# Kernel optimization log

Measured on AMD Instinct MI355X. Metric: run time of the kernel, lower is better.

## Reference

```python
import jax, jax.numpy as jnp
import numpy as np

WS = 7
NUM_HEADS = 12
DIM = 384
HEAD_DIM = DIM // NUM_HEADS
SCALE = HEAD_DIM ** -0.5


def _rel_pos_index(ws: int) -> jnp.ndarray:
    coords = np.stack(np.meshgrid(np.arange(ws), np.arange(ws), indexing='ij'))  # (2, ws, ws)
    cf = coords.reshape(2, -1)                       # (2, ws*ws)
    rel = cf[:, :, None] - cf[:, None, :]            # (2, N, N)
    rel = rel.transpose(1, 2, 0).copy()              # (N, N, 2)
    rel[..., 0] += ws - 1
    rel[..., 1] += ws - 1
    rel[..., 0] *= 2 * ws - 1
    return jnp.asarray(rel.sum(-1))                  # (N, N) int indices into bias table


REL_IDX = _rel_pos_index(WS)


def setup_inputs() -> dict:
    key = jax.random.key(0)
    ks = jax.random.split(key, 7)
    BW, N, C = 4096, WS * WS, DIM
    num_win = 64
    return {
        'x': jax.random.normal(ks[0], (BW, N, C), jnp.float32),
        'mask': jax.random.normal(ks[1], (num_win, N, N), jnp.float32),
        'qkv_w': jax.random.normal(ks[2], (3 * C, C), jnp.float32) * 0.02,
        'qkv_b': jax.random.normal(ks[3], (3 * C,), jnp.float32) * 0.02,
        'proj_w': jax.random.normal(ks[4], (C, C), jnp.float32) * 0.02,
        'proj_b': jax.random.normal(ks[5], (C,), jnp.float32) * 0.02,
        'bias_table': jax.random.normal(ks[6], ((2 * WS - 1) ** 2, NUM_HEADS), jnp.float32) * 0.02,
    }


def reference(x, mask, qkv_w, qkv_b, proj_w, proj_b, bias_table):
    BW, N, C = x.shape
    H, hd = NUM_HEADS, HEAD_DIM
    # QKV projection: (BW, N, 3C) -> (3, BW, H, N, hd)
    qkv = (x @ qkv_w.T + qkv_b).reshape(BW, N, 3, H, hd).transpose(2, 0, 3, 1, 4)
    q, k, v = qkv[0], qkv[1], qkv[2]
    attn = jnp.einsum('bhnd,bhmd->bhnm', q, k) * SCALE  # (BW, H, N, N)
    bias = bias_table[REL_IDX]                          # (N, N, H)
    attn = attn + bias.transpose(2, 0, 1)[None]
    num_win = mask.shape[0]
    attn = attn.reshape(BW // num_win, num_win, H, N, N) + mask[None, :, None]
    attn = attn.reshape(BW, H, N, N)
    attn = jax.nn.softmax(attn, axis=-1)
    out = jnp.einsum('bhnm,bhmd->bhnd', attn, v)        # (BW, H, N, hd)
    out = out.transpose(0, 2, 1, 3).reshape(BW, N, C)
    return out @ proj_w.T + proj_b
```

## Files before the change

kernel.cpp:

```cpp
#include <hip/hip_runtime.h>

typedef unsigned short u16;
typedef unsigned int u32;
typedef __attribute__((ext_vector_type(8))) short short8;
typedef __attribute__((ext_vector_type(4))) float floatx4;

#define SCALE_Q 0.17677669529663687f

__device__ __forceinline__ u16 f2bf(float f) {
  u32 u = __float_as_uint(f);
  u = (u + 0x7fffu + ((u >> 16) & 1u)) >> 16;
  return (u16)u;
}

__device__ __forceinline__ void gload_lds16(const void* g, void* l) {
  __builtin_amdgcn_global_load_lds(
      (const __attribute__((address_space(1))) u32*)g,
      (__attribute__((address_space(3))) u32*)l, 16, 0, 0);
}

__device__ __forceinline__ floatx4 mfma16(short8 a, short8 b, floatx4 c) {
  return __builtin_amdgcn_mfma_f32_16x16x32_bf16(a, b, c, 0, 0, 0);
}

__global__ void cast_w_kernel(const float* __restrict__ qkv_w,
                              const float* __restrict__ proj_w,
                              u16* __restrict__ wb1, u16* __restrict__ wb2) {
  int idx = blockIdx.x * 256 + threadIdx.x;
  wb1[idx] = f2bf(qkv_w[idx]);
  if (idx < 147456) wb2[idx] = f2bf(proj_w[idx]);
}

__global__ __launch_bounds__(256) void cast_x_kernel(const float* __restrict__ x,
                                                     u16* __restrict__ xb) {
  const size_t i = ((size_t)blockIdx.x * 256 + threadIdx.x) * 8;
  const float4 f0 = *(const float4*)(x + i);
  const float4 f1 = *(const float4*)(x + i + 4);
  uint4 pk;
  pk.x = (u32)f2bf(f0.x) | ((u32)f2bf(f0.y) << 16);
  pk.y = (u32)f2bf(f0.z) | ((u32)f2bf(f0.w) << 16);
  pk.z = (u32)f2bf(f1.x) | ((u32)f2bf(f1.y) << 16);
  pk.w = (u32)f2bf(f1.z) | ((u32)f2bf(f1.w) << 16);
  *(uint4*)(xb + i) = pk;
}

__global__ void comb_kernel(const float* __restrict__ bias_table,
                            const float* __restrict__ mask,
                            float* __restrict__ comb) {
  int wh = blockIdx.x;
  int w = wh / 12, h = wh - w * 12;
  float* dst = comb + (size_t)wh * 4096;
  for (int e = threadIdx.x; e < 4096; e += 256) {
    int q = e >> 6, p = e & 63;
    float v;
    if (q >= 49) v = -1e30f;
    else if (p >= 49) v = 0.0f;
    else {
      int pi = p / 7, pj = p - pi * 7;
      int qi = q / 7, qj = q - qi * 7;
      int ridx = (pi - qi + 6) * 13 + (pj - qj + 6);
      v = bias_table[ridx * 12 + h] + mask[(size_t)w * 2401 + p * 49 + q];
    }
    dst[e] = v;
  }
}

__global__ __launch_bounds__(256) void qkv_gemm(const u16* __restrict__ A,
                                                const u16* __restrict__ B,
                                                const float* __restrict__ bias,
                                                u16* __restrict__ C) {
  __shared__ u16 As[2][4096];
  __shared__ u16 Bs[2][4096];
  const int tid = threadIdx.x;
  const int lane = tid & 63;
  const int wave = tid >> 6;
  const int l15 = lane & 15;
  const int quad = lane >> 4;
  const int wr = wave >> 1, wc = wave & 1;
  const u32 bid = blockIdx.x;
  const u32 xcd = bid & 7;
  const u32 slot = bid >> 3;
  const u32 grp = slot / 9;
  const u32 tn = slot - grp * 9;
  const u32 tm = xcd * 196 + grp;

  const int c0 = tid, c1 = tid + 256;
  const int m0 = c0 >> 2, kp0 = (c0 & 3) ^ ((m0 >> 1) & 3);
  const int m1 = c1 >> 2, kp1 = (c1 & 3) ^ ((m1 >> 1) & 3);
  const u16* Ab0 = A + (size_t)(tm * 128 + m0) * 384 + kp0 * 8;
  const u16* Ab1 = A + (size_t)(tm * 128 + m1) * 384 + kp1 * 8;
  const u16* Bb0 = B + (size_t)(tn * 128 + m0) * 384 + kp0 * 8;
  const u16* Bb1 = B + (size_t)(tn * 128 + m1) * 384 + kp1 * 8;
  const int ld0 = c0 * 8, ld1 = c1 * 8;

  floatx4 acc[4][4];
#pragma unroll
  for (int i = 0; i < 4; ++i)
#pragma unroll
    for (int j = 0; j < 4; ++j) acc[i][j] = (floatx4){0.f, 0.f, 0.f, 0.f};

#define QSTAGE(buf, k0)                       \
  do {                                        \
    gload_lds16(Ab0 + (k0), &As[buf][ld0]);   \
    gload_lds16(Ab1 + (k0), &As[buf][ld1]);   \
    gload_lds16(Bb0 + (k0), &Bs[buf][ld0]);   \
    gload_lds16(Bb1 + (k0), &Bs[buf][ld1]);   \
  } while (0)

  QSTAGE(0, 0);
  __syncthreads();

  const int xq = quad ^ ((l15 >> 1) & 3);
  const int abase = (wr * 64 + l15) * 32 + xq * 8;
  const int bbase = (wc * 64 + l15) * 32 + xq * 8;
  for (int kb = 0; kb < 12; ++kb) {
    const int cur = kb & 1;
    if (kb < 11) QSTAGE(cur ^ 1, (kb + 1) * 32);
    short8 af[4], bfr[4];
#pragma unroll
    for (int i = 0; i < 4; ++i)
      af[i] = *(const short8*)(&As[cur][abase + i * 512]);
#pragma unroll
    for (int i = 0; i < 4; ++i)
      bfr[i] = *(const short8*)(&Bs[cur][bbase + i * 512]);
#pragma unroll
    for (int mi = 0; mi < 4; ++mi)
#pragma unroll
      for (int ni = 0; ni < 4; ++ni)
        acc[mi][ni] = mfma16(af[mi], bfr[ni], acc[mi][ni]);
    if (kb < 11) __syncthreads();
  }
#undef QSTAGE

#pragma unroll
  for (int ni = 0; ni < 4; ++ni) {
    const int gbase = (int)tn * 128 + wc * 64 + ni * 16;
    const int which = gbase / 384;
    const int rem = gbase - which * 384;
    const int h = rem >> 5;
    const int db = rem & 31;
    const float bb = bias[gbase + l15];
    const float scale = (which == 0) ? SCALE_Q : 1.0f;
    u16* hp = C + ((size_t)which * 49152 + h) * 1568 + db + l15;
#pragma unroll
    for (int mi = 0; mi < 4; ++mi) {
      const int grow0 = (int)tm * 128 + wr * 64 + mi * 16 + quad * 4;
#pragma unroll
      for (int r = 0; r < 4; ++r) {
        const int grow = grow0 + r;
        const int b = grow / 49;
        const int tok = grow - b * 49;
        hp[(size_t)b * 18816 + tok * 32] = f2bf((acc[mi][ni][r] + bb) * scale);
      }
    }
  }
}

__global__ __launch_bounds__(64) void attn_kernel(const u16* __restrict__ qkv,
                                                  const float* __restrict__ comb,
                                                  u16* __restrict__ ao) {
  __shared__ uint4 smem4[864];
  u16* Ps = (u16*)smem4;
  u16* Vt = (u16*)((char*)smem4 + 9216);

  const int tid = threadIdx.x;
  const int l15 = tid & 15, quad = tid >> 4;
  const int bh = blockIdx.x;
  const int b = bh / 12, h = bh - b * 12;
  const int w = b & 63;

  const size_t hoff = (size_t)bh * 1568;
  const u16* qb = qkv + hoff;
  const u16* kbp = qkv + (size_t)49152 * 1568 + hoff;
  const u16* vb = qkv + (size_t)98304 * 1568 + hoff;

  short8 aq[4], bk[4];
  const short8 z8 = {0, 0, 0, 0, 0, 0, 0, 0};
#pragma unroll
  for (int i = 0; i < 3; ++i) {
    aq[i] = *(const short8*)(qb + (i * 16 + l15) * 32 + quad * 8);
    bk[i] = *(const short8*)(kbp + (i * 16 + l15) * 32 + quad * 8);
  }
  aq[3] = (l15 == 0) ? *(const short8*)(qb + 48 * 32 + quad * 8) : z8;
  bk[3] = (l15 == 0) ? *(const short8*)(kbp + 48 * 32 + quad * 8) : z8;

  const uint4 z = make_uint4(0u, 0u, 0u, 0u);
  for (int i = tid; i < 288; i += 64) smem4[576 + i] = z;

  for (int s0 = tid; s0 < 196; s0 += 64) {
    const int t = s0 >> 2, part = s0 & 3;
    const uint4 dv = *(const uint4*)(vb + t * 32 + part * 8);
    const int d0 = part * 8;
    const u32 vv[4] = {dv.x, dv.y, dv.z, dv.w};
#pragma unroll
    for (int j = 0; j < 4; ++j) {
      Vt[(d0 + 2 * j) * 72 + t] = (u16)(vv[j] & 0xffffu);
      Vt[(d0 + 2 * j + 1) * 72 + t] = (u16)(vv[j] >> 16);
    }
  }

  floatx4 s[4][4];
  const floatx4 z4 = (floatx4){0.f, 0.f, 0.f, 0.f};
  __builtin_amdgcn_s_setprio(1);
#pragma unroll
  for (int mi = 0; mi < 4; ++mi)
#pragma unroll
    for (int ni = 0; ni < 4; ++ni) s[mi][ni] = mfma16(aq[mi], bk[ni], z4);
  __builtin_amdgcn_s_setprio(0);

  const float* cb = comb + (size_t)(w * 12 + h) * 4096;
#pragma unroll
  for (int ni = 0; ni < 4; ++ni)
#pragma unroll
    for (int mi = 0; mi < 4; ++mi) {
      const float4 cv = *(const float4*)(cb + (ni * 16 + l15) * 64 + mi * 16 + quad * 4);
      s[mi][ni][0] += cv.x;
      s[mi][ni][1] += cv.y;
      s[mi][ni][2] += cv.z;
      s[mi][ni][3] += cv.w;
    }

  floatx4 mx[4], sm[4];
#pragma unroll
  for (int mi = 0; mi < 4; ++mi)
#pragma unroll
    for (int r = 0; r < 4; ++r)
      mx[mi][r] = fmaxf(fmaxf(s[mi][0][r], s[mi][1][r]), fmaxf(s[mi][2][r], s[mi][3][r]));
#pragma unroll
  for (int d = 1; d < 16; d <<= 1)
#pragma unroll
    for (int mi = 0; mi < 4; ++mi)
#pragma unroll
      for (int r = 0; r < 4; ++r)
        mx[mi][r] = fmaxf(mx[mi][r], __shfl_xor(mx[mi][r], d));
#pragma unroll
  for (int mi = 0; mi < 4; ++mi)
#pragma unroll
    for (int r = 0; r < 4; ++r) {
      float a = 0.f;
#pragma unroll
      for (int ni = 0; ni < 4; ++ni) {
        const float e = __expf(s[mi][ni][r] - mx[mi][r]);
        s[mi][ni][r] = e;
        a += e;
      }
      sm[mi][r] = a;
    }
#pragma unroll
  for (int d = 1; d < 16; d <<= 1)
#pragma unroll
    for (int mi = 0; mi < 4; ++mi)
#pragma unroll
      for (int r = 0; r < 4; ++r)
        sm[mi][r] += __shfl_xor(sm[mi][r], d);

#pragma unroll
  for (int mi = 0; mi < 4; ++mi)
#pragma unroll
    for (int r = 0; r < 4; ++r) {
      const float rinv = 1.0f / sm[mi][r];
      const int row = mi * 16 + quad * 4 + r;
#pragma unroll
      for (int ni = 0; ni < 4; ++ni)
        Ps[row * 72 + ni * 16 + l15] = f2bf(s[mi][ni][r] * rinv);
    }
  __syncthreads();

  floatx4 o[4][2];
#pragma unroll
  for (int mi = 0; mi < 4; ++mi)
#pragma unroll
    for (int ni = 0; ni < 2; ++ni) o[mi][ni] = z4;
#pragma unroll
  for (int kk = 0; kk < 2; ++kk) {
    short8 ap[4], bv[2];
#pragma unroll
    for (int mi = 0; mi < 4; ++mi)
      ap[mi] = *(const short8*)(Ps + (mi * 16 + l15) * 72 + kk * 32 + quad * 8);
#pragma unroll
    for (int ni = 0; ni < 2; ++ni)
      bv[ni] = *(const short8*)(Vt + (ni * 16 + l15) * 72 + kk * 32 + quad * 8);
    __builtin_amdgcn_s_setprio(1);
#pragma unroll
    for (int mi = 0; mi < 4; ++mi)
#pragma unroll
      for (int ni = 0; ni < 2; ++ni) o[mi][ni] = mfma16(ap[mi], bv[ni], o[mi][ni]);
    __builtin_amdgcn_s_setprio(0);
  }
#pragma unroll
  for (int mi = 0; mi < 4; ++mi)
#pragma unroll
    for (int r = 0; r < 4; ++r) {
      const int row = mi * 16 + quad * 4 + r;
      if (row < 49) {
        u16* dst = ao + (size_t)(b * 49 + row) * 384 + h * 32;
#pragma unroll
        for (int ni = 0; ni < 2; ++ni)
          dst[ni * 16 + l15] = f2bf(o[mi][ni][r]);
      }
    }
}

__global__ __launch_bounds__(256) void proj_gemm(const u16* __restrict__ A,
                                                 const u16* __restrict__ B,
                                                 const float* __restrict__ bias,
                                                 float* __restrict__ C) {
  __shared__ u16 As[2][4096];
  __shared__ u16 Bs[2][4096];
  const int tid = threadIdx.x;
  const int lane = tid & 63;
  const int wave = tid >> 6;
  const int l15 = lane & 15;
  const int quad = lane >> 4;
  const int wr = wave >> 1, wc = wave & 1;
  const u32 bid = blockIdx.x;
  const u32 xcd = bid & 7;
  const u32 slot = bid >> 3;
  const u32 grp = slot / 3;
  const u32 tn = slot - grp * 3;
  const u32 tm = xcd * 196 + grp;

  const int c0 = tid, c1 = tid + 256;
  const int m0 = c0 >> 2, kp0 = (c0 & 3) ^ ((m0 >> 1) & 3);
  const int m1 = c1 >> 2, kp1 = (c1 & 3) ^ ((m1 >> 1) & 3);
  const u16* Ab0 = A + (size_t)(tm * 128 + m0) * 384 + kp0 * 8;
  const u16* Ab1 = A + (size_t)(tm * 128 + m1) * 384 + kp1 * 8;
  const u16* Bb0 = B + (size_t)(tn * 128 + m0) * 384 + kp0 * 8;
  const u16* Bb1 = B + (size_t)(tn * 128 + m1) * 384 + kp1 * 8;
  const int ld0 = c0 * 8, ld1 = c1 * 8;

  floatx4 acc[4][4];
#pragma unroll
  for (int i = 0; i < 4; ++i)
#pragma unroll
    for (int j = 0; j < 4; ++j) acc[i][j] = (floatx4){0.f, 0.f, 0.f, 0.f};

#define PSTAGE(buf, k0)                       \
  do {                                        \
    gload_lds16(Ab0 + (k0), &As[buf][ld0]);   \
    gload_lds16(Ab1 + (k0), &As[buf][ld1]);   \
    gload_lds16(Bb0 + (k0), &Bs[buf][ld0]);   \
    gload_lds16(Bb1 + (k0), &Bs[buf][ld1]);   \
  } while (0)

  PSTAGE(0, 0);
  __syncthreads();

  const int xq = quad ^ ((l15 >> 1) & 3);
  const int abase = (wr * 64 + l15) * 32 + xq * 8;
  const int bbase = (wc * 64 + l15) * 32 + xq * 8;
  for (int kb = 0; kb < 12; ++kb) {
    const int cur = kb & 1;
    if (kb < 11) PSTAGE(cur ^ 1, (kb + 1) * 32);
    short8 af[4], bfr[4];
#pragma unroll
    for (int i = 0; i < 4; ++i)
      af[i] = *(const short8*)(&As[cur][abase + i * 512]);
#pragma unroll
    for (int i = 0; i < 4; ++i)
      bfr[i] = *(const short8*)(&Bs[cur][bbase + i * 512]);
#pragma unroll
    for (int mi = 0; mi < 4; ++mi)
#pragma unroll
      for (int ni = 0; ni < 4; ++ni)
        acc[mi][ni] = mfma16(af[mi], bfr[ni], acc[mi][ni]);
    if (kb < 11) __syncthreads();
  }
#undef PSTAGE

#pragma unroll
  for (int ni = 0; ni < 4; ++ni) {
    const int gcol = tn * 128 + wc * 64 + ni * 16 + l15;
    const float bb = bias[gcol];
#pragma unroll
    for (int mi = 0; mi < 4; ++mi) {
      const int grow0 = tm * 128 + wr * 64 + mi * 16 + quad * 4;
#pragma unroll
      for (int r = 0; r < 4; ++r)
        C[(size_t)(grow0 + r) * 384 + gcol] = acc[mi][ni][r] + bb;
    }
  }
}

extern "C" void kernel_launch(void* const* d_in, const int* in_sizes, int n_in,
                              void* d_out, int out_size, void* d_ws, size_t ws_size,
                              hipStream_t stream) {
  const float* x = (const float*)d_in[0];
  const float* mask = (const float*)d_in[1];
  const float* qkv_w = (const float*)d_in[2];
  const float* qkv_b = (const float*)d_in[3];
  const float* proj_w = (const float*)d_in[4];
  const float* proj_b = (const float*)d_in[5];
  const float* bias_table = (const float*)d_in[6];
  float* out = (float*)d_out;
  char* ws = (char*)d_ws;

  u16* wb1 = (u16*)(ws);
  u16* wb2 = (u16*)(ws + 884736);
  float* comb = (float*)(ws + 1179648);
  u16* qkvb = (u16*)(ws + 13762560);
  u16* ao = (u16*)(ws + 476184576);
  u16* xb = ao;

  hipLaunchKernelGGL(cast_w_kernel, dim3(1728), dim3(256), 0, stream, qkv_w, proj_w, wb1, wb2);
  hipLaunchKernelGGL(cast_x_kernel, dim3(37632), dim3(256), 0, stream, x, xb);
  hipLaunchKernelGGL(comb_kernel, dim3(768), dim3(256), 0, stream, bias_table, mask, comb);
  hipLaunchKernelGGL(qkv_gemm, dim3(14112), dim3(256), 0, stream, xb, wb1, qkv_b, qkvb);
  hipLaunchKernelGGL(attn_kernel, dim3(49152), dim3(64), 0, stream, qkvb, comb, ao);
  hipLaunchKernelGGL(proj_gemm, dim3(4704), dim3(256), 0, stream, ao, wb2, proj_b, out);
}
```

Baseline: 1.208 ms.

## Fuse window attention with output projection and single-buffer the QKV GEMM

The separate per-head attention kernel and the projection GEMM are replaced by one kernel per window. Its four waves each handle three heads, write the attention output into a shared-memory tile, then run the projection against weights read straight from global memory. This removes the global round trip of the attention output and one launch. In exchange it uses about 105KB of LDS with launch bounds of one block, so occupancy is low and the weight loads in the projection loop are poorly hidden. Separately, the QKV GEMM drops its double buffering for a single LDS buffer synchronised before and after compute, which halves its LDS but exposes load latency.

```diff
diff --git a/kernel.cpp b/kernel.cpp
--- a/kernel.cpp
+++ b/kernel.cpp
@@ -69,8 +69,8 @@
                                                 const u16* __restrict__ B,
                                                 const float* __restrict__ bias,
                                                 u16* __restrict__ C) {
-  __shared__ u16 As[2][4096];
-  __shared__ u16 Bs[2][4096];
+  __shared__ u16 As[4096];
+  __shared__ u16 Bs[4096];
   const int tid = threadIdx.x;
   const int lane = tid & 63;
   const int wave = tid >> 6;
@@ -99,38 +99,30 @@
 #pragma unroll
     for (int j = 0; j < 4; ++j) acc[i][j] = (floatx4){0.f, 0.f, 0.f, 0.f};
 
-#define QSTAGE(buf, k0)                       \
-  do {                                        \
-    gload_lds16(Ab0 + (k0), &As[buf][ld0]);   \
-    gload_lds16(Ab1 + (k0), &As[buf][ld1]);   \
-    gload_lds16(Bb0 + (k0), &Bs[buf][ld0]);   \
-    gload_lds16(Bb1 + (k0), &Bs[buf][ld1]);   \
-  } while (0)
-
-  QSTAGE(0, 0);
-  __syncthreads();
-
   const int xq = quad ^ ((l15 >> 1) & 3);
   const int abase = (wr * 64 + l15) * 32 + xq * 8;
   const int bbase = (wc * 64 + l15) * 32 + xq * 8;
   for (int kb = 0; kb < 12; ++kb) {
-    const int cur = kb & 1;
-    if (kb < 11) QSTAGE(cur ^ 1, (kb + 1) * 32);
+    const int k0 = kb * 32;
+    gload_lds16(Ab0 + k0, &As[ld0]);
+    gload_lds16(Ab1 + k0, &As[ld1]);
+    gload_lds16(Bb0 + k0, &Bs[ld0]);
+    gload_lds16(Bb1 + k0, &Bs[ld1]);
+    __syncthreads();
     short8 af[4], bfr[4];
 #pragma unroll
     for (int i = 0; i < 4; ++i)
-      af[i] = *(const short8*)(&As[cur][abase + i * 512]);
+      af[i] = *(const short8*)(&As[abase + i * 512]);
 #pragma unroll
     for (int i = 0; i < 4; ++i)
-      bfr[i] = *(const short8*)(&Bs[cur][bbase + i * 512]);
+      bfr[i] = *(const short8*)(&Bs[bbase + i * 512]);
 #pragma unroll
     for (int mi = 0; mi < 4; ++mi)
 #pragma unroll
       for (int ni = 0; ni < 4; ++ni)
         acc[mi][ni] = mfma16(af[mi], bfr[ni], acc[mi][ni]);
-    if (kb < 11) __syncthreads();
-  }
-#undef QSTAGE
+    __syncthreads();
+  }
 
 #pragma unroll
   for (int ni = 0; ni < 4; ++ni) {
@@ -156,229 +148,198 @@
   }
 }
 
-__global__ __launch_bounds__(64) void attn_kernel(const u16* __restrict__ qkv,
-                                                  const float* __restrict__ comb,
-                                                  u16* __restrict__ ao) {
-  __shared__ uint4 smem4[864];
-  u16* Ps = (u16*)smem4;
-  u16* Vt = (u16*)((char*)smem4 + 9216);
-
-  const int tid = threadIdx.x;
-  const int l15 = tid & 15, quad = tid >> 4;
-  const int bh = blockIdx.x;
-  const int b = bh / 12, h = bh - b * 12;
-  const int w = b & 63;
-
-  const size_t hoff = (size_t)bh * 1568;
-  const u16* qb = qkv + hoff;
-  const u16* kbp = qkv + (size_t)49152 * 1568 + hoff;
-  const u16* vb = qkv + (size_t)98304 * 1568 + hoff;
-
-  short8 aq[4], bk[4];
-  const short8 z8 = {0, 0, 0, 0, 0, 0, 0, 0};
-#pragma unroll
-  for (int i = 0; i < 3; ++i) {
-    aq[i] = *(const short8*)(qb + (i * 16 + l15) * 32 + quad * 8);
-    bk[i] = *(const short8*)(kbp + (i * 16 + l15) * 32 + quad * 8);
-  }
-  aq[3] = (l15 == 0) ? *(const short8*)(qb + 48 * 32 + quad * 8) : z8;
-  bk[3] = (l15 == 0) ? *(const short8*)(kbp + 48 * 32 + quad * 8) : z8;
-
-  const uint4 z = make_uint4(0u, 0u, 0u, 0u);
-  for (int i = tid; i < 288; i += 64) smem4[576 + i] = z;
-
-  for (int s0 = tid; s0 < 196; s0 += 64) {
-    const int t = s0 >> 2, part = s0 & 3;
-    const uint4 dv = *(const uint4*)(vb + t * 32 + part * 8);
-    const int d0 = part * 8;
-    const u32 vv[4] = {dv.x, dv.y, dv.z, dv.w};
-#pragma unroll
-    for (int j = 0; j < 4; ++j) {
-      Vt[(d0 + 2 * j) * 72 + t] = (u16)(vv[j] & 0xffffu);
-      Vt[(d0 + 2 * j + 1) * 72 + t] = (u16)(vv[j] >> 16);
-    }
-  }
-
-  floatx4 s[4][4];
-  const floatx4 z4 = (floatx4){0.f, 0.f, 0.f, 0.f};
-  __builtin_amdgcn_s_setprio(1);
-#pragma unroll
-  for (int mi = 0; mi < 4; ++mi)
-#pragma unroll
-    for (int ni = 0; ni < 4; ++ni) s[mi][ni] = mfma16(aq[mi], bk[ni], z4);
-  __builtin_amdgcn_s_setprio(0);
-
-  const float* cb = comb + (size_t)(w * 12 + h) * 4096;
-#pragma unroll
-  for (int ni = 0; ni < 4; ++ni)
-#pragma unroll
-    for (int mi = 0; mi < 4; ++mi) {
-      const float4 cv = *(const float4*)(cb + (ni * 16 + l15) * 64 + mi * 16 + quad * 4);
-      s[mi][ni][0] += cv.x;
-      s[mi][ni][1] += cv.y;
-      s[mi][ni][2] += cv.z;
-      s[mi][ni][3] += cv.w;
-    }
-
-  floatx4 mx[4], sm[4];
-#pragma unroll
-  for (int mi = 0; mi < 4; ++mi)
-#pragma unroll
-    for (int r = 0; r < 4; ++r)
-      mx[mi][r] = fmaxf(fmaxf(s[mi][0][r], s[mi][1][r]), fmaxf(s[mi][2][r], s[mi][3][r]));
-#pragma unroll
-  for (int d = 1; d < 16; d <<= 1)
-#pragma unroll
-    for (int mi = 0; mi < 4; ++mi)
-#pragma unroll
-      for (int r = 0; r < 4; ++r)
-        mx[mi][r] = fmaxf(mx[mi][r], __shfl_xor(mx[mi][r], d));
-#pragma unroll
-  for (int mi = 0; mi < 4; ++mi)
-#pragma unroll
-    for (int r = 0; r < 4; ++r) {
-      float a = 0.f;
-#pragma unroll
-      for (int ni = 0; ni < 4; ++ni) {
-        const float e = __expf(s[mi][ni][r] - mx[mi][r]);
-        s[mi][ni][r] = e;
-        a += e;
-      }
-      sm[mi][r] = a;
-    }
-#pragma unroll
-  for (int d = 1; d < 16; d <<= 1)
-#pragma unroll
-    for (int mi = 0; mi < 4; ++mi)
-#pragma unroll
-      for (int r = 0; r < 4; ++r)
-        sm[mi][r] += __shfl_xor(sm[mi][r], d);
-
-#pragma unroll
-  for (int mi = 0; mi < 4; ++mi)
-#pragma unroll
-    for (int r = 0; r < 4; ++r) {
-      const float rinv = 1.0f / sm[mi][r];
-      const int row = mi * 16 + quad * 4 + r;
-#pragma unroll
-      for (int ni = 0; ni < 4; ++ni)
-        Ps[row * 72 + ni * 16 + l15] = f2bf(s[mi][ni][r] * rinv);
-    }
-  __syncthreads();
-
-  floatx4 o[4][2];
-#pragma unroll
-  for (int mi = 0; mi < 4; ++mi)
-#pragma unroll
-    for (int ni = 0; ni < 2; ++ni) o[mi][ni] = z4;
-#pragma unroll
-  for (int kk = 0; kk < 2; ++kk) {
-    short8 ap[4], bv[2];
-#pragma unroll
-    for (int mi = 0; mi < 4; ++mi)
-      ap[mi] = *(const short8*)(Ps + (mi * 16 + l15) * 72 + kk * 32 + quad * 8);
-#pragma unroll
-    for (int ni = 0; ni < 2; ++ni)
-      bv[ni] = *(const short8*)(Vt + (ni * 16 + l15) * 72 + kk * 32 + quad * 8);
-    __builtin_amdgcn_s_setprio(1);
-#pragma unroll
-    for (int mi = 0; mi < 4; ++mi)
-#pragma unroll
-      for (int ni = 0; ni < 2; ++ni) o[mi][ni] = mfma16(ap[mi], bv[ni], o[mi][ni]);
-    __builtin_amdgcn_s_setprio(0);
-  }
-#pragma unroll
-  for (int mi = 0; mi < 4; ++mi)
-#pragma unroll
-    for (int r = 0; r < 4; ++r) {
-      const int row = mi * 16 + quad * 4 + r;
-      if (row < 49) {
-        u16* dst = ao + (size_t)(b * 49 + row) * 384 + h * 32;
-#pragma unroll
-        for (int ni = 0; ni < 2; ++ni)
-          dst[ni * 16 + l15] = f2bf(o[mi][ni][r]);
-      }
-    }
-}
-
-__global__ __launch_bounds__(256) void proj_gemm(const u16* __restrict__ A,
-                                                 const u16* __restrict__ B,
-                                                 const float* __restrict__ bias,
-                                                 float* __restrict__ C) {
-  __shared__ u16 As[2][4096];
-  __shared__ u16 Bs[2][4096];
+__global__ __launch_bounds__(256, 1) void attn_proj(const u16* __restrict__ qkv,
+                                                    const float* __restrict__ comb,
+                                                    const u16* __restrict__ pw,
+                                                    const float* __restrict__ pb,
+                                                    float* __restrict__ out) {
+  __shared__ uint4 smem[6592];
+  u16* aoS = (u16*)smem;
   const int tid = threadIdx.x;
   const int lane = tid & 63;
-  const int wave = tid >> 6;
-  const int l15 = lane & 15;
-  const int quad = lane >> 4;
-  const int wr = wave >> 1, wc = wave & 1;
-  const u32 bid = blockIdx.x;
-  const u32 xcd = bid & 7;
-  const u32 slot = bid >> 3;
-  const u32 grp = slot / 3;
-  const u32 tn = slot - grp * 3;
-  const u32 tm = xcd * 196 + grp;
-
-  const int c0 = tid, c1 = tid + 256;
-  const int m0 = c0 >> 2, kp0 = (c0 & 3) ^ ((m0 >> 1) & 3);
-  const int m1 = c1 >> 2, kp1 = (c1 & 3) ^ ((m1 >> 1) & 3);
-  const u16* Ab0 = A + (size_t)(tm * 128 + m0) * 384 + kp0 * 8;
-  const u16* Ab1 = A + (size_t)(tm * 128 + m1) * 384 + kp1 * 8;
-  const u16* Bb0 = B + (size_t)(tn * 128 + m0) * 384 + kp0 * 8;
-  const u16* Bb1 = B + (size_t)(tn * 128 + m1) * 384 + kp1 * 8;
-  const int ld0 = c0 * 8, ld1 = c1 * 8;
-
-  floatx4 acc[4][4];
-#pragma unroll
-  for (int i = 0; i < 4; ++i)
-#pragma unroll
-    for (int j = 0; j < 4; ++j) acc[i][j] = (floatx4){0.f, 0.f, 0.f, 0.f};
-
-#define PSTAGE(buf, k0)                       \
-  do {                                        \
-    gload_lds16(Ab0 + (k0), &As[buf][ld0]);   \
-    gload_lds16(Ab1 + (k0), &As[buf][ld1]);   \
-    gload_lds16(Bb0 + (k0), &Bs[buf][ld0]);   \
-    gload_lds16(Bb1 + (k0), &Bs[buf][ld1]);   \
-  } while (0)
-
-  PSTAGE(0, 0);
+  const int wv = tid >> 6;
+  const int l15 = lane & 15, quad = lane >> 4;
+  u16* Ps = (u16*)((char*)smem + 50176 + wv * 9216);
+  u16* Vt = (u16*)((char*)smem + 87040 + wv * 4608);
+
+  const int bid = blockIdx.x;
+  const int w = bid >> 6;
+  const int b = (bid & 63) * 64 + w;
+
+  {
+    uint4* v4 = (uint4*)Vt;
+    const uint4 zz = make_uint4(0u, 0u, 0u, 0u);
+    for (int i = lane; i < 288; i += 64) v4[i] = zz;
+  }
+
+  const floatx4 z4 = (floatx4){0.f, 0.f, 0.f, 0.f};
+  const short8 z8 = {0, 0, 0, 0, 0, 0, 0, 0};
+
+  for (int hi = 0; hi < 3; ++hi) {
+    const int h = wv + hi * 4;
+    const size_t hoff = (size_t)(b * 12 + h) * 1568;
+    const u16* qb = qkv + hoff;
+    const u16* kbp = qkv + (size_t)49152 * 1568 + hoff;
+    const u16* vb = qkv + (size_t)98304 * 1568 + hoff;
+
+    short8 aq[4], bk[4];
+#pragma unroll
+    for (int i = 0; i < 3; ++i) {
+      aq[i] = *(const short8*)(qb + (i * 16 + l15) * 32 + quad * 8);
+      bk[i] = *(const short8*)(kbp + (i * 16 + l15) * 32 + quad * 8);
+    }
+    aq[3] = (l15 == 0) ? *(const short8*)(qb + 48 * 32 + quad * 8) : z8;
+    bk[3] = (l15 == 0) ? *(const short8*)(kbp + 48 * 32 + quad * 8) : z8;
+
+    for (int s0 = lane; s0 < 196; s0 += 64) {
+      const int t = s0 >> 2, part = s0 & 3;
+      const uint4 dv = *(const uint4*)(vb + t * 32 + part * 8);
+      const int d0 = part * 8;
+      const u32 vv[4] = {dv.x, dv.y, dv.z, dv.w};
+#pragma unroll
+      for (int e = 0; e < 4; ++e) {
+        Vt[(d0 + 2 * e) * 72 + t] = (u16)(vv[e] & 0xffffu);
+        Vt[(d0 + 2 * e + 1) * 72 + t] = (u16)(vv[e] >> 16);
+      }
+    }
+
+    floatx4 s[4][4];
+    __builtin_amdgcn_s_setprio(1);
+#pragma unroll
+    for (int mi = 0; mi < 4; ++mi)
+#pragma unroll
+      for (int ni = 0; ni < 4; ++ni) s[mi][ni] = mfma16(aq[mi], bk[ni], z4);
+    __builtin_amdgcn_s_setprio(0);
+
+    const float* cb = comb + (size_t)(w * 12 + h) * 4096;
+#pragma unroll
+    for (int ni = 0; ni < 4; ++ni)
+#pragma unroll
+      for (int mi = 0; mi < 4; ++mi) {
+        const float4 cv = *(const float4*)(cb + (ni * 16 + l15) * 64 + mi * 16 + quad * 4);
+        s[mi][ni][0] += cv.x;
+        s[mi][ni][1] += cv.y;
+        s[mi][ni][2] += cv.z;
+        s[mi][ni][3] += cv.w;
+      }
+
+    floatx4 mx[4], sm[4];
+#pragma unroll
+    for (int mi = 0; mi < 4; ++mi)
+#pragma unroll
+      for (int r = 0; r < 4; ++r)
+        mx[mi][r] = fmaxf(fmaxf(s[mi][0][r], s[mi][1][r]), fmaxf(s[mi][2][r], s[mi][3][r]));
+#pragma unroll
+    for (int d = 1; d < 16; d <<= 1)
+#pragma unroll
+      for (int mi = 0; mi < 4; ++mi)
+#pragma unroll
+        for (int r = 0; r < 4; ++r)
+          mx[mi][r] = fmaxf(mx[mi][r], __shfl_xor(mx[mi][r], d));
+#pragma unroll
+    for (int mi = 0; mi < 4; ++mi)
+#pragma unroll
+      for (int r = 0; r < 4; ++r) {
+        float a = 0.f;
+#pragma unroll
+        for (int ni = 0; ni < 4; ++ni) {
+          const float e = __expf(s[mi][ni][r] - mx[mi][r]);
+          s[mi][ni][r] = e;
+          a += e;
+        }
+        sm[mi][r] = a;
+      }
+#pragma unroll
+    for (int d = 1; d < 16; d <<= 1)
+#pragma unroll
+      for (int mi = 0; mi < 4; ++mi)
+#pragma unroll
+        for (int r = 0; r < 4; ++r)
+          sm[mi][r] += __shfl_xor(sm[mi][r], d);
+
+#pragma unroll
+    for (int mi = 0; mi < 4; ++mi)
+#pragma unroll
+      for (int r = 0; r < 4; ++r) {
+        const float rinv = 1.0f / sm[mi][r];
+        const int row = mi * 16 + quad * 4 + r;
+#pragma unroll
+        for (int ni = 0; ni < 4; ++ni)
+          Ps[row * 72 + ni * 16 + l15] = f2bf(s[mi][ni][r] * rinv);
+      }
+    __syncthreads();
+
+    floatx4 o[4][2];
+#pragma unroll
+    for (int mi = 0; mi < 4; ++mi)
+#pragma unroll
+      for (int ni = 0; ni < 2; ++ni) o[mi][ni] = z4;
+#pragma unroll
+    for (int kk = 0; kk < 2; ++kk) {
+      short8 ap[4], bv[2];
+#pragma unroll
+      for (int mi = 0; mi < 4; ++mi)
+        ap[mi] = *(const short8*)(Ps + (mi * 16 + l15) * 72 + kk * 32 + quad * 8);
+#pragma unroll
+      for (int ni = 0; ni < 2; ++ni)
+        bv[ni] = *(const short8*)(Vt + (ni * 16 + l15) * 72 + kk * 32 + quad * 8);
+      __builtin_amdgcn_s_setprio(1);
+#pragma unroll
+      for (int mi = 0; mi < 4; ++mi)
+#pragma unroll
+        for (int ni = 0; ni < 2; ++ni) o[mi][ni] = mfma16(ap[mi], bv[ni], o[mi][ni]);
+      __builtin_amdgcn_s_setprio(0);
+    }
+#pragma unroll
+    for (int mi = 0; mi < 4; ++mi)
+#pragma unroll
+      for (int r = 0; r < 4; ++r) {
+        const int row = mi * 16 + quad * 4 + r;
+#pragma unroll
+        for (int ni = 0; ni < 2; ++ni)
+          aoS[row * 392 + h * 32 + ni * 16 + l15] = f2bf(o[mi][ni][r]);
+      }
+  }
+
   __syncthreads();
 
-  const int xq = quad ^ ((l15 >> 1) & 3);
-  const int abase = (wr * 64 + l15) * 32 + xq * 8;
-  const int bbase = (wc * 64 + l15) * 32 + xq * 8;
+  floatx4 pacc[4][6];
+#pragma unroll
+  for (int mi = 0; mi < 4; ++mi)
+#pragma unroll
+    for (int nf = 0; nf < 6; ++nf) pacc[mi][nf] = z4;
+
+  const u16* pwb = pw + (size_t)(wv * 96 + l15) * 384 + quad * 8;
+#pragma unroll
   for (int kb = 0; kb < 12; ++kb) {
-    const int cur = kb & 1;
-    if (kb < 11) PSTAGE(cur ^ 1, (kb + 1) * 32);
-    short8 af[4], bfr[4];
-#pragma unroll
-    for (int i = 0; i < 4; ++i)
-      af[i] = *(const short8*)(&As[cur][abase + i * 512]);
-#pragma unroll
-    for (int i = 0; i < 4; ++i)
-      bfr[i] = *(const short8*)(&Bs[cur][bbase + i * 512]);
-#pragma unroll
-    for (int mi = 0; mi < 4; ++mi)
-#pragma unroll
-      for (int ni = 0; ni < 4; ++ni)
-        acc[mi][ni] = mfma16(af[mi], bfr[ni], acc[mi][ni]);
-    if (kb < 11) __syncthreads();
-  }
-#undef PSTAGE
-
-#pragma unroll
-  for (int ni = 0; ni < 4; ++ni) {
-    const int gcol = tn * 128 + wc * 64 + ni * 16 + l15;
-    const float bb = bias[gcol];
-#pragma unroll
-    for (int mi = 0; mi < 4; ++mi) {
-      const int grow0 = tm * 128 + wr * 64 + mi * 16 + quad * 4;
-#pragma unroll
-      for (int r = 0; r < 4; ++r)
-        C[(size_t)(grow0 + r) * 384 + gcol] = acc[mi][ni][r] + bb;
-    }
+    short8 paf[4], pbf[6];
+#pragma unroll
+    for (int mi = 0; mi < 4; ++mi)
+      paf[mi] = *(const short8*)(aoS + (mi * 16 + l15) * 392 + kb * 32 + quad * 8);
+#pragma unroll
+    for (int nf = 0; nf < 6; ++nf)
+      pbf[nf] = *(const short8*)(pwb + nf * 6144 + kb * 32);
+    __builtin_amdgcn_s_setprio(1);
+#pragma unroll
+    for (int mi = 0; mi < 4; ++mi)
+#pragma unroll
+      for (int nf = 0; nf < 6; ++nf)
+        pacc[mi][nf] = mfma16(paf[mi], pbf[nf], pacc[mi][nf]);
+    __builtin_amdgcn_s_setprio(0);
+  }
+
+#pragma unroll
+  for (int nf = 0; nf < 6; ++nf) {
+    const int col = wv * 96 + nf * 16 + l15;
+    const float bb = pb[col];
+#pragma unroll
+    for (int mi = 0; mi < 4; ++mi)
+#pragma unroll
+      for (int r = 0; r < 4; ++r) {
+        const int row = mi * 16 + quad * 4 + r;
+        if (row < 49)
+          out[((size_t)b * 49 + row) * 384 + col] = pacc[mi][nf][r] + bb;
+      }
   }
 }
 
@@ -399,13 +360,11 @@
   u16* wb2 = (u16*)(ws + 884736);
   float* comb = (float*)(ws + 1179648);
   u16* qkvb = (u16*)(ws + 13762560);
-  u16* ao = (u16*)(ws + 476184576);
-  u16* xb = ao;
+  u16* xb = (u16*)(ws + 476184576);
 
   hipLaunchKernelGGL(cast_w_kernel, dim3(1728), dim3(256), 0, stream, qkv_w, proj_w, wb1, wb2);
   hipLaunchKernelGGL(cast_x_kernel, dim3(37632), dim3(256), 0, stream, x, xb);
   hipLaunchKernelGGL(comb_kernel, dim3(768), dim3(256), 0, stream, bias_table, mask, comb);
   hipLaunchKernelGGL(qkv_gemm, dim3(14112), dim3(256), 0, stream, xb, wb1, qkv_b, qkvb);
-  hipLaunchKernelGGL(attn_kernel, dim3(49152), dim3(64), 0, stream, qkvb, comb, ao);
-  hipLaunchKernelGGL(proj_gemm, dim3(4704), dim3(256), 0, stream, ao, wb2, proj_b, out);
-}
+  hipLaunchKernelGGL(attn_proj, dim3(4096), dim3(256), 0, stream, qkvb, comb, wb2, proj_b, out);
+}
```

New measurement: 1.426 ms. 18.1% more time.
